# Kernel tuning notes

Measured on AMD Instinct MI355X. Metric: run time of the kernel, lower is better.

The kernel has to match this reference:

```python
import jax, jax.numpy as jnp
import numpy as np

V = 512          # vocab_size (= input_size = hidden_size of LSTMCell)
L = 128          # formula_max_len
PAD_ID = 0
SOS_ID = 1


def setup_inputs() -> dict:
    key = jax.random.key(0)
    k1, k2, k3, k4, k5 = jax.random.split(key, 5)
    B = 512
    s = 1.0 / np.sqrt(V)  # torch LSTMCell init scale
    return {
        "x": jax.random.normal(k1, (B, V), dtype=jnp.float32),
        "W_ih": jax.random.uniform(k2, (4 * V, V), jnp.float32, -s, s),
        "W_hh": jax.random.uniform(k3, (4 * V, V), jnp.float32, -s, s),
        "b_ih": jax.random.uniform(k4, (4 * V,), jnp.float32, -s, s),
        "b_hh": jax.random.uniform(k5, (4 * V,), jnp.float32, -s, s),
    }


def _decode(x, W_ih, W_hh, b_ih, b_hh):
    B = x.shape[0]
    dt = x.dtype
    sos = jax.nn.one_hot(SOS_ID, V, dtype=dt)
    pad = jax.nn.one_hot(PAD_ID, V, dtype=dt)

    h0 = x                      # hidden_state = x.squeeze()
    c0 = jnp.zeros_like(x)
    inp0 = jnp.broadcast_to(sos, (B, V))

    def step(carry, _):
        h, c, inp = carry
        # torch LSTMCell: gates = x W_ih^T + b_ih + h W_hh^T + b_hh, order i,f,g,o
        gates = inp @ W_ih.T + b_ih + h @ W_hh.T + b_hh   # [B, 4V]
        i, f, g, o = jnp.split(gates, 4, axis=-1)
        c_new = jax.nn.sigmoid(f) * c + jax.nn.sigmoid(i) * jnp.tanh(g)
        h_new = jax.nn.sigmoid(o) * jnp.tanh(c_new)
        probas = jax.nn.softmax(h_new, axis=-1)           # [B, V]
        nxt = jax.nn.one_hot(jnp.argmax(probas, axis=-1), V, dtype=dt)
        return (h_new, c_new, nxt), probas

    _, probas_seq = jax.lax.scan(step, (h0, c0, inp0), None, length=L - 1)
    # probas_seq: [L-1, B, V] -> [B, L-1, V]; last position stays PAD one-hot
    preds = jnp.swapaxes(probas_seq, 0, 1)
    pad_row = jnp.broadcast_to(pad, (B, 1, V))
    return jnp.concatenate([preds, pad_row], axis=1)      # [B, L, V]


def reference(x, W_ih, W_hh, b_ih, b_hh):
    return _decode(x, W_ih, W_hh, b_ih, b_hh)
```

## Files before the change

kernel.cpp:

```cpp
#include <hip/hip_runtime.h>

#define VSZ 512
#define LSEQ 128
#define NTHR 512
#define NBLK 256
#define NGRP 8
#define GBLK 32
#define SPIN_MAX  (1u << 20)
#define SPIN_STEP (1u << 17)

using short8  = __attribute__((ext_vector_type(8))) short;
using short4v = __attribute__((ext_vector_type(4))) short;
using floatx4 = __attribute__((ext_vector_type(4))) float;
using ull2v   = __attribute__((ext_vector_type(2))) unsigned long long;

static __device__ __forceinline__ short f2bf(float f) {
    union { float f; unsigned u; } v; v.f = f;
    unsigned u = v.u;
    unsigned r = (u + 0x7fffu + ((u >> 16) & 1u)) >> 16;
    return (short)r;
}
static __device__ __forceinline__ float bf2f(short s) {
    union { unsigned u; float f; } v; v.u = ((unsigned)(unsigned short)s) << 16;
    return v.f;
}
static __device__ __forceinline__ float fast_rcp(float x) { return __builtin_amdgcn_rcpf(x); }
static __device__ __forceinline__ float sigm(float x)   { return fast_rcp(1.0f + __expf(-x)); }
static __device__ __forceinline__ float tanh_f(float x) { return 1.0f - 2.0f * fast_rcp(__expf(2.0f * x) + 1.0f); }

template<bool F> static __device__ __forceinline__ void ldx4f(floatx4& d, const float* p) {
    if constexpr (F) asm volatile("global_load_dwordx4 %0, %1, off sc0"     : "=v"(d) : "v"(p));
    else             asm volatile("global_load_dwordx4 %0, %1, off sc0 sc1" : "=v"(d) : "v"(p));
}
template<bool F> static __device__ __forceinline__ void ldx4u(ull2v& d, const unsigned long long* p) {
    if constexpr (F) asm volatile("global_load_dwordx4 %0, %1, off sc0"     : "=v"(d) : "v"(p));
    else             asm volatile("global_load_dwordx4 %0, %1, off sc0 sc1" : "=v"(d) : "v"(p));
}
template<bool F> static __device__ __forceinline__ void ldx4s(short8& d, const short* p) {
    if constexpr (F) asm volatile("global_load_dwordx4 %0, %1, off sc0"     : "=v"(d) : "v"(p));
    else             asm volatile("global_load_dwordx4 %0, %1, off sc0 sc1" : "=v"(d) : "v"(p));
}
template<bool F> static __device__ __forceinline__ void stg16(void* p, unsigned v) {
    if constexpr (F) asm volatile("global_store_short %0, %1, off sc0"     :: "v"(p), "v"(v) : "memory");
    else             asm volatile("global_store_short %0, %1, off sc0 sc1" :: "v"(p), "v"(v) : "memory");
}
template<bool F> static __device__ __forceinline__ void stg32(void* p, unsigned v) {
    if constexpr (F) asm volatile("global_store_dword %0, %1, off sc0"     :: "v"(p), "v"(v) : "memory");
    else             asm volatile("global_store_dword %0, %1, off sc0 sc1" :: "v"(p), "v"(v) : "memory");
}
template<bool F> static __device__ __forceinline__ void stg64(void* p, unsigned long long v) {
    if constexpr (F) asm volatile("global_store_dwordx2 %0, %1, off sc0"     :: "v"(p), "v"(v) : "memory");
    else             asm volatile("global_store_dwordx2 %0, %1, off sc0 sc1" :: "v"(p), "v"(v) : "memory");
}

static __device__ __forceinline__ unsigned atomic_add_dev(unsigned* p, unsigned v) {
    unsigned old;
    asm volatile("global_atomic_add %0, %1, %2, off sc0 sc1\n\ts_waitcnt vmcnt(0)"
                 : "=v"(old) : "v"(p), "v"(v) : "memory");
    return old;
}
static __device__ __forceinline__ unsigned ld_dev_u32(const unsigned* p) {
    unsigned v;
    asm volatile("global_load_dword %0, %1, off sc0 sc1\n\ts_waitcnt vmcnt(0)"
                 : "=v"(v) : "v"(p) : "memory");
    return v;
}

static __device__ __forceinline__ void step_arrive(unsigned* cnt, int tid) {
    asm volatile("s_waitcnt vmcnt(0)" ::: "memory");
    __builtin_amdgcn_s_barrier();
    if (tid == 0) atomic_add_dev(cnt, 1u);
}
static __device__ __forceinline__ void step_wait(unsigned* cnt, int t, int tid) {
    if (tid == 0) {
        const unsigned target = (unsigned)(GBLK * (t + 1));
        unsigned it = 0;
        while (ld_dev_u32(cnt) < target) {
            if (++it > SPIN_STEP) break;
            if (it > 16) __builtin_amdgcn_s_sleep(1);
        }
    }
    __builtin_amdgcn_s_barrier();
}

static __device__ __forceinline__ void grid_barrier_dev(unsigned* ctrl, int tid, int bid) {
    asm volatile("s_waitcnt vmcnt(0)" ::: "memory");
    __builtin_amdgcn_s_barrier();
    if (tid == 0) {
        unsigned* l1   = ctrl + 256 + (bid >> 4) * 32;
        unsigned* root = ctrl + 768;
        unsigned* gen  = ctrl + 800;
        unsigned old = atomic_add_dev(l1, 1u);
        if ((old & 15) == 15) {
            unsigned rold = atomic_add_dev(root, 1u);
            if ((rold & 15) == 15) atomic_add_dev(gen, 1u);
        }
        unsigned it = 0;
        while (ld_dev_u32(gen) < 1u) {
            if (++it > SPIN_MAX) break;
            __builtin_amdgcn_s_sleep(1);
        }
    }
    __builtin_amdgcn_s_barrier();
}

__global__ void prep_wb(const float* __restrict__ Whh, short* __restrict__ Wb) {
    int tid = threadIdx.x;
    int lane = tid & 63;
    int T = blockIdx.x * 8 + (tid >> 6);
    int g  = T & 3;
    int k  = (T >> 2) & 15;
    int vt = T >> 6;
    int l15 = lane & 15, lg = lane >> 4;
    const float* src = Whh + (size_t)(g * 512 + vt * 16 + l15) * 512 + k * 32 + lg * 8;
    short8 o;
#pragma unroll
    for (int i = 0; i < 8; ++i) o[i] = f2bf(src[i]);
    *(short8*)(Wb + (size_t)T * 512 + lane * 8) = o;
}

__global__ void prep_wxb(const float* __restrict__ Wih, const float* __restrict__ bih,
                         const float* __restrict__ bhh, short* __restrict__ Wxb) {
    __shared__ float tile[64][65];
    int j0 = blockIdx.x * 64;
    int a0 = blockIdx.y * 64;
    int tid = threadIdx.x;
    for (int i = tid; i < 4096; i += NTHR) {
        int r = i >> 6, c = i & 63;
        int jj = j0 + r;
        tile[r][c] = Wih[(size_t)jj * 512 + a0 + c] + bih[jj] + bhh[jj];
    }
    __syncthreads();
    int v0 = j0 & 511;
    for (int i = tid; i < 4096; i += NTHR) {
        int r = i >> 6, c = i & 63;
        Wxb[(((size_t)(a0 + r)) * 512 + v0 + c) * 4 + (j0 >> 9)] = f2bf(tile[c][r]);
    }
}

template<bool F>
static __device__ __forceinline__ void run_decoder(
    const float* __restrict__ x, const short* __restrict__ Wb, const short* __restrict__ Wxb,
    float* __restrict__ out,
    short* hbuf, float* psum, unsigned long long* pmax, unsigned* cnt,
    short (*hlds)[520], float (*gl)[4][17], float* rinvL, int* aidL,
    int tid, int g, int j) {

    const int lane = tid & 63;
    const int w    = tid >> 6;
    const int l15  = lane & 15;
    const int lg   = lane >> 4;
    const int v16  = tid & 15;
    const int rr   = tid >> 4;
    const int row0g = g * 64;
    const int jv   = j * 16 + v16;
    const int mt = w >> 1, g0 = (w & 1) * 2;

    short8 bb[16][2];
#pragma unroll
    for (int kc = 0; kc < 16; ++kc) {
        const short* p = Wb + ((size_t)j * 64 + kc * 4 + g0) * 512 + lane * 8;
        asm volatile("global_load_dwordx4 %0, %1, off"             : "=v"(bb[kc][0]) : "v"(p));
        asm volatile("global_load_dwordx4 %0, %1, off offset:1024" : "=v"(bb[kc][1]) : "v"(p));
    }
    asm volatile("s_waitcnt vmcnt(0)" ::: "memory");
    __builtin_amdgcn_sched_barrier(0);

    float cst[2] = {0.f, 0.f};
    float exv[2] = {0.f, 0.f};

    for (int t = 0; t < LSEQ - 1; ++t) {
        if (t == 0) {
            if (tid < 64) aidL[tid] = 1;
#pragma unroll
            for (int p = 0; p < 8; ++p) {
                int row = (tid >> 6) + 8 * p;
                const float* src = x + (size_t)(row0g + row) * VSZ + (tid & 63) * 8;
                short8 v;
#pragma unroll
                for (int e = 0; e < 8; ++e) v[e] = f2bf(src[e]);
                *(short8*)&hlds[row][(tid & 63) * 8] = v;
            }
        } else {
            const int tb2 = (t + 1) & 1;
            floatx4 s4v; ull2v m2a, m2b;
            const float* ps = psum + ((size_t)tb2 * 512 + row0g) * 32 + tid * 4;
            const unsigned long long* pm = pmax + ((size_t)tb2 * 512 + row0g) * 32 + tid * 4;
            ldx4f<F>(s4v, ps);
            ldx4u<F>(m2a, pm);
            ldx4u<F>(m2b, pm + 2);
            short8 stg[8];
            const short* hsrc = hbuf + (size_t)tb2 * (VSZ * VSZ);
#pragma unroll
            for (int p = 0; p < 8; ++p) {
                int row = (tid >> 6) + 8 * p;
                ldx4s<F>(stg[p], hsrc + (size_t)(row0g + row) * VSZ + (tid & 63) * 8);
            }
            asm volatile("s_waitcnt vmcnt(8)" ::: "memory");
            __builtin_amdgcn_sched_barrier(0);
            float s = (s4v[0] + s4v[1]) + (s4v[2] + s4v[3]);
            unsigned long long m = m2a[0] > m2a[1] ? m2a[0] : m2a[1];
            unsigned long long m2 = m2b[0] > m2b[1] ? m2b[0] : m2b[1];
            if (m2 > m) m = m2;
#pragma unroll
            for (int d = 1; d < 8; d <<= 1) {
                s += __shfl_xor(s, d);
                unsigned long long mo = __shfl_xor(m, d);
                if (mo > m) m = mo;
            }
            if ((tid & 7) == 0) {
                int r = tid >> 3;
                rinvL[r] = 1.0f / s;
                aidL[r]  = (int)(~(unsigned)m);
            }
            asm volatile("s_waitcnt vmcnt(0)" ::: "memory");
            __builtin_amdgcn_sched_barrier(0);
#pragma unroll
            for (int p = 0; p < 8; ++p) {
                int row = (tid >> 6) + 8 * p;
                *(short8*)&hlds[row][(tid & 63) * 8] = stg[p];
            }
        }
        __syncthreads();

        short4v wxv0, wxv1;
        {
            const short* gp0 = Wxb + ((size_t)aidL[rr]      * VSZ + jv) * 4;
            const short* gp1 = Wxb + ((size_t)aidL[rr + 32] * VSZ + jv) * 4;
            asm volatile("global_load_dwordx2 %0, %1, off" : "=v"(wxv0) : "v"(gp0));
            asm volatile("global_load_dwordx2 %0, %1, off" : "=v"(wxv1) : "v"(gp1));
        }

        floatx4 a0v = {0,0,0,0}, a1v = {0,0,0,0};
#pragma unroll
        for (int kc = 0; kc < 16; ++kc) {
            short8 av = *(const short8*)&hlds[mt * 16 + l15][kc * 32 + lg * 8];
            a0v = __builtin_amdgcn_mfma_f32_16x16x32_bf16(av, bb[kc][0], a0v, 0, 0, 0);
            a1v = __builtin_amdgcn_mfma_f32_16x16x32_bf16(av, bb[kc][1], a1v, 0, 0, 0);
        }
#pragma unroll
        for (int q = 0; q < 4; ++q) {
            gl[mt * 16 + lg * 4 + q][g0][l15]     = a0v[q];
            gl[mt * 16 + lg * 4 + q][g0 + 1][l15] = a1v[q];
        }
        __syncthreads();

        asm volatile("s_waitcnt vmcnt(0)" ::: "memory");
        __builtin_amdgcn_sched_barrier(0);
        float pex0 = exv[0], pex1 = exv[1];
#pragma unroll
        for (int s2 = 0; s2 < 2; ++s2) {
            int r = rr + 32 * s2;
            short4v wxv = s2 ? wxv1 : wxv0;
            float gi = gl[r][0][v16] + bf2f(wxv[0]);
            float gf = gl[r][1][v16] + bf2f(wxv[1]);
            float gg = gl[r][2][v16] + bf2f(wxv[2]);
            float go = gl[r][3][v16] + bf2f(wxv[3]);
            float cn = sigm(gf) * cst[s2] + sigm(gi) * tanh_f(gg);
            cst[s2] = cn;
            float hn = sigm(go) * tanh_f(cn);
            stg16<F>(hbuf + (size_t)(t & 1) * (VSZ * VSZ) + (size_t)(row0g + r) * VSZ + jv,
                     (unsigned)(unsigned short)f2bf(hn));
            float e = __expf(hn);
            exv[s2] = e;
            float s = e; float mv = e; int mi = jv;
#pragma unroll
            for (int m = 1; m < 16; m <<= 1) {
                s += __shfl_xor(s, m);
                float mv2 = __shfl_xor(mv, m);
                int   mi2 = __shfl_xor(mi, m);
                if (mv2 > mv || (mv2 == mv && mi2 < mi)) { mv = mv2; mi = mi2; }
            }
            if (v16 == 0) {
                size_t o32 = ((size_t)(t & 1) * 512 + row0g + r) * 32 + j;
                unsigned long long pk =
                    ((unsigned long long)__float_as_uint(mv) << 32) | (unsigned)(~(unsigned)mi);
                stg32<F>(psum + o32, __float_as_uint(s));
                stg64<F>(pmax + o32, pk);
            }
        }

        step_arrive(cnt, tid);
        if (t > 0) {
            __builtin_nontemporal_store(pex0 * rinvL[rr],
                &out[((size_t)(row0g + rr) * LSEQ + (t - 1)) * VSZ + jv]);
            __builtin_nontemporal_store(pex1 * rinvL[rr + 32],
                &out[((size_t)(row0g + rr + 32) * LSEQ + (t - 1)) * VSZ + jv]);
        }
        step_wait(cnt, t, tid);
    }

    {
        floatx4 s4v;
        ldx4f<F>(s4v, psum + (size_t)row0g * 32 + tid * 4);
        asm volatile("s_waitcnt vmcnt(0)" ::: "memory");
        __builtin_amdgcn_sched_barrier(0);
        float s = (s4v[0] + s4v[1]) + (s4v[2] + s4v[3]);
#pragma unroll
        for (int d = 1; d < 8; d <<= 1) s += __shfl_xor(s, d);
        if ((tid & 7) == 0) rinvL[tid >> 3] = 1.0f / s;
    }
    __syncthreads();
#pragma unroll
    for (int s2 = 0; s2 < 2; ++s2) {
        int r = rr + 32 * s2;
        __builtin_nontemporal_store(exv[s2] * rinvL[r],
            &out[((size_t)(row0g + r) * LSEQ + (LSEQ - 2)) * VSZ + jv]);
        __builtin_nontemporal_store((jv == 0) ? 1.0f : 0.0f,
            &out[((size_t)(row0g + r) * LSEQ + (LSEQ - 1)) * VSZ + jv]);
    }
}

__launch_bounds__(NTHR, 2)
__global__ void decoder_coop(const float* __restrict__ x, const short* __restrict__ Wb,
                             const short* __restrict__ Wxb,
                             short* hbuf_s, float* psum_s, unsigned long long* pmax_s,
                             short* hbuf_f, float* psum_f, unsigned long long* pmax_f,
                             unsigned* ctrl, float* __restrict__ out, int allow_fast) {
    __shared__ short hlds[64][520];
    __shared__ float gl[64][4][17];
    __shared__ float rinvL[64];
    __shared__ int   aidL[64];
    __shared__ int   sh_xcc, sh_slot, sh_ok;
    __shared__ unsigned sh_cnts[NGRP];

    const int tid = threadIdx.x;
    const int bid = blockIdx.x;

    if (tid == 0) {
        unsigned xcc;
        asm volatile("s_getreg_b32 %0, hwreg(HW_REG_XCC_ID)" : "=s"(xcc));
        xcc &= 7;
        unsigned slot = atomic_add_dev(ctrl + xcc * 32, 1u);
        sh_xcc = (int)xcc; sh_slot = (int)slot;
    }
    grid_barrier_dev(ctrl, tid, bid);
    if (tid < NGRP) sh_cnts[tid] = ld_dev_u32(ctrl + tid * 32);
    __syncthreads();
    if (tid == 0) {
        int ok = allow_fast && (sh_slot < GBLK);
#pragma unroll
        for (int g = 0; g < NGRP; ++g) ok = ok && (sh_cnts[g] == GBLK);
        sh_ok = ok;
    }
    __syncthreads();
    const int ok = sh_ok;
    const int g = ok ? sh_xcc : (bid & 7);
    const int j = ok ? sh_slot : (bid >> 3);
    unsigned* cnt = ctrl + 1024 + g * 64;

    if (ok)
        run_decoder<true >(x, Wb, Wxb, out, hbuf_f, psum_f, pmax_f, cnt,
                           hlds, gl, rinvL, aidL, tid, g, j);
    else
        run_decoder<false>(x, Wb, Wxb, out, hbuf_s, psum_s, pmax_s, cnt,
                           hlds, gl, rinvL, aidL, tid, g, j);
}

extern "C" void kernel_launch(void* const* d_in, const int* in_sizes, int n_in,
                              void* d_out, int out_size, void* d_ws, size_t ws_size,
                              hipStream_t stream) {
    const float* x    = (const float*)d_in[0];
    const float* W_ih = (const float*)d_in[1];
    const float* W_hh = (const float*)d_in[2];
    const float* b_ih = (const float*)d_in[3];
    const float* b_hh = (const float*)d_in[4];

    char* ws = (char*)d_ws;
    short* Wb     = (short*)ws;
    short* Wxb    = (short*)(ws + (2u << 20));
    short* hbuf_s = (short*)(ws + (4u << 20));
    float* psum_s = (float*)(ws + (5u << 20));
    unsigned long long* pmax_s = (unsigned long long*)(ws + (5u << 20) + (128u << 10));
    unsigned* ctrl = (unsigned*)(ws + (5u << 20) + (384u << 10));
    short* hbuf_f = (short*)(ws + (5u << 20) + (400u << 10));
    float* psum_f = (float*)(ws + (6u << 20) + (400u << 10));
    unsigned long long* pmax_f = (unsigned long long*)(ws + (6u << 20) + (528u << 10));
    const size_t needed = (6ull << 20) + (784ull << 10);
    int allow_fast = (ws_size >= needed) ? 1 : 0;

    prep_wb<<<256, NTHR, 0, stream>>>(W_hh, Wb);
    prep_wxb<<<dim3(32, 8), NTHR, 0, stream>>>(W_ih, b_ih, b_hh, Wxb);
    hipMemsetAsync(ctrl, 0, 16384, stream);

    float* outp = (float*)d_out;
    void* args[] = { (void*)&x, (void*)&Wb, (void*)&Wxb,
                     (void*)&hbuf_s, (void*)&psum_s, (void*)&pmax_s,
                     (void*)&hbuf_f, (void*)&psum_f, (void*)&pmax_f,
                     (void*)&ctrl, (void*)&outp, (void*)&allow_fast };
    hipLaunchCooperativeKernel((const void*)decoder_coop, dim3(NBLK), dim3(NTHR),
                               args, 0, stream);
}
```

Baseline: 639.0 us.

## Add 256-thread, 512-block decoder variant with 16 row groups per step

```diff
diff --git a/kernel.cpp b/kernel.cpp
--- a/kernel.cpp
+++ b/kernel.cpp
@@ -2,9 +2,7 @@
 
 #define VSZ 512
 #define LSEQ 128
-#define NTHR 512
-#define NBLK 256
-#define NGRP 8
+#define PREPTHR 512
 #define GBLK 32
 #define SPIN_MAX  (1u << 20)
 #define SPIN_STEP (1u << 17)
@@ -83,17 +81,18 @@
     __builtin_amdgcn_s_barrier();
 }
 
+template<int NL1>
 static __device__ __forceinline__ void grid_barrier_dev(unsigned* ctrl, int tid, int bid) {
     asm volatile("s_waitcnt vmcnt(0)" ::: "memory");
     __builtin_amdgcn_s_barrier();
     if (tid == 0) {
         unsigned* l1   = ctrl + 256 + (bid >> 4) * 32;
-        unsigned* root = ctrl + 768;
-        unsigned* gen  = ctrl + 800;
+        unsigned* root = ctrl + 256 + NL1 * 32;
+        unsigned* gen  = root + 32;
         unsigned old = atomic_add_dev(l1, 1u);
         if ((old & 15) == 15) {
             unsigned rold = atomic_add_dev(root, 1u);
-            if ((rold & 15) == 15) atomic_add_dev(gen, 1u);
+            if ((rold & (NL1 - 1)) == (unsigned)(NL1 - 1)) atomic_add_dev(gen, 1u);
         }
         unsigned it = 0;
         while (ld_dev_u32(gen) < 1u) {
@@ -125,21 +124,21 @@
     int j0 = blockIdx.x * 64;
     int a0 = blockIdx.y * 64;
     int tid = threadIdx.x;
-    for (int i = tid; i < 4096; i += NTHR) {
+    for (int i = tid; i < 4096; i += PREPTHR) {
         int r = i >> 6, c = i & 63;
         int jj = j0 + r;
         tile[r][c] = Wih[(size_t)jj * 512 + a0 + c] + bih[jj] + bhh[jj];
     }
     __syncthreads();
     int v0 = j0 & 511;
-    for (int i = tid; i < 4096; i += NTHR) {
+    for (int i = tid; i < 4096; i += PREPTHR) {
         int r = i >> 6, c = i & 63;
         Wxb[(((size_t)(a0 + r)) * 512 + v0 + c) * 4 + (j0 >> 9)] = f2bf(tile[c][r]);
     }
 }
 
 template<bool F>
-static __device__ __forceinline__ void run_decoder(
+static __device__ __forceinline__ void run_decoder512(
     const float* __restrict__ x, const short* __restrict__ Wb, const short* __restrict__ Wxb,
     float* __restrict__ out,
     short* hbuf, float* psum, unsigned long long* pmax, unsigned* cnt,
@@ -311,18 +310,18 @@
     }
 }
 
-__launch_bounds__(NTHR, 2)
-__global__ void decoder_coop(const float* __restrict__ x, const short* __restrict__ Wb,
-                             const short* __restrict__ Wxb,
-                             short* hbuf_s, float* psum_s, unsigned long long* pmax_s,
-                             short* hbuf_f, float* psum_f, unsigned long long* pmax_f,
-                             unsigned* ctrl, float* __restrict__ out, int allow_fast) {
+__launch_bounds__(512, 2)
+__global__ void decoder_coop512(const float* __restrict__ x, const short* __restrict__ Wb,
+                                const short* __restrict__ Wxb,
+                                short* hbuf_s, float* psum_s, unsigned long long* pmax_s,
+                                short* hbuf_f, float* psum_f, unsigned long long* pmax_f,
+                                unsigned* ctrl, float* __restrict__ out, int allow_fast) {
     __shared__ short hlds[64][520];
     __shared__ float gl[64][4][17];
     __shared__ float rinvL[64];
     __shared__ int   aidL[64];
     __shared__ int   sh_xcc, sh_slot, sh_ok;
-    __shared__ unsigned sh_cnts[NGRP];
+    __shared__ unsigned sh_cnts[8];
 
     const int tid = threadIdx.x;
     const int bid = blockIdx.x;
@@ -334,27 +333,246 @@
         unsigned slot = atomic_add_dev(ctrl + xcc * 32, 1u);
         sh_xcc = (int)xcc; sh_slot = (int)slot;
     }
-    grid_barrier_dev(ctrl, tid, bid);
-    if (tid < NGRP) sh_cnts[tid] = ld_dev_u32(ctrl + tid * 32);
+    grid_barrier_dev<16>(ctrl, tid, bid);
+    if (tid < 8) sh_cnts[tid] = ld_dev_u32(ctrl + tid * 32);
     __syncthreads();
     if (tid == 0) {
         int ok = allow_fast && (sh_slot < GBLK);
 #pragma unroll
-        for (int g = 0; g < NGRP; ++g) ok = ok && (sh_cnts[g] == GBLK);
+        for (int g = 0; g < 8; ++g) ok = ok && (sh_cnts[g] == GBLK);
         sh_ok = ok;
     }
     __syncthreads();
     const int ok = sh_ok;
     const int g = ok ? sh_xcc : (bid & 7);
     const int j = ok ? sh_slot : (bid >> 3);
-    unsigned* cnt = ctrl + 1024 + g * 64;
+    unsigned* cnt = ctrl + 2048 + g * 64;
 
     if (ok)
-        run_decoder<true >(x, Wb, Wxb, out, hbuf_f, psum_f, pmax_f, cnt,
-                           hlds, gl, rinvL, aidL, tid, g, j);
+        run_decoder512<true >(x, Wb, Wxb, out, hbuf_f, psum_f, pmax_f, cnt,
+                              hlds, gl, rinvL, aidL, tid, g, j);
     else
-        run_decoder<false>(x, Wb, Wxb, out, hbuf_s, psum_s, pmax_s, cnt,
-                           hlds, gl, rinvL, aidL, tid, g, j);
+        run_decoder512<false>(x, Wb, Wxb, out, hbuf_s, psum_s, pmax_s, cnt,
+                              hlds, gl, rinvL, aidL, tid, g, j);
+}
+
+template<bool F>
+static __device__ __forceinline__ void run_decoder256(
+    const float* __restrict__ x, const short* __restrict__ Wb, const short* __restrict__ Wxb,
+    float* __restrict__ out,
+    short* hbuf, float* psum, unsigned long long* pmax, unsigned* cnt,
+    short (*hlds)[520], float (*gl)[4][17], float* rinvL, int* aidL,
+    int tid, int g, int j) {
+
+    const int lane = tid & 63;
+    const int w    = tid >> 6;
+    const int l15  = lane & 15;
+    const int lg   = lane >> 4;
+    const int v16  = tid & 15;
+    const int rr   = tid >> 4;
+    const int row0g = g * 32;
+    const int jv   = j * 16 + v16;
+    const int mt = w >> 1, g0 = (w & 1) * 2;
+
+    short8 bb[16][2];
+#pragma unroll
+    for (int kc = 0; kc < 16; ++kc) {
+        const short* p = Wb + ((size_t)j * 64 + kc * 4 + g0) * 512 + lane * 8;
+        asm volatile("global_load_dwordx4 %0, %1, off"             : "=v"(bb[kc][0]) : "v"(p));
+        asm volatile("global_load_dwordx4 %0, %1, off offset:1024" : "=v"(bb[kc][1]) : "v"(p));
+    }
+    asm volatile("s_waitcnt vmcnt(0)" ::: "memory");
+    __builtin_amdgcn_sched_barrier(0);
+
+    float cst[2] = {0.f, 0.f};
+    float exv[2] = {0.f, 0.f};
+
+    for (int t = 0; t < LSEQ - 1; ++t) {
+        if (t == 0) {
+            if (tid < 32) aidL[tid] = 1;
+#pragma unroll
+            for (int p = 0; p < 8; ++p) {
+                int row = (tid >> 6) + 4 * p;
+                const float* src = x + (size_t)(row0g + row) * VSZ + (tid & 63) * 8;
+                short8 v;
+#pragma unroll
+                for (int e = 0; e < 8; ++e) v[e] = f2bf(src[e]);
+                *(short8*)&hlds[row][(tid & 63) * 8] = v;
+            }
+        } else {
+            const int tb2 = (t + 1) & 1;
+            floatx4 s4v; ull2v m2a, m2b;
+            const float* ps = psum + ((size_t)tb2 * 512 + row0g) * 32 + tid * 4;
+            const unsigned long long* pm = pmax + ((size_t)tb2 * 512 + row0g) * 32 + tid * 4;
+            ldx4f<F>(s4v, ps);
+            ldx4u<F>(m2a, pm);
+            ldx4u<F>(m2b, pm + 2);
+            short8 stg[8];
+            const short* hsrc = hbuf + (size_t)tb2 * (VSZ * VSZ);
+#pragma unroll
+            for (int p = 0; p < 8; ++p) {
+                int row = (tid >> 6) + 4 * p;
+                ldx4s<F>(stg[p], hsrc + (size_t)(row0g + row) * VSZ + (tid & 63) * 8);
+            }
+            asm volatile("s_waitcnt vmcnt(8)" ::: "memory");
+            __builtin_amdgcn_sched_barrier(0);
+            float s = (s4v[0] + s4v[1]) + (s4v[2] + s4v[3]);
+            unsigned long long m = m2a[0] > m2a[1] ? m2a[0] : m2a[1];
+            unsigned long long m2 = m2b[0] > m2b[1] ? m2b[0] : m2b[1];
+            if (m2 > m) m = m2;
+#pragma unroll
+            for (int d = 1; d < 8; d <<= 1) {
+                s += __shfl_xor(s, d);
+                unsigned long long mo = __shfl_xor(m, d);
+                if (mo > m) m = mo;
+            }
+            if ((tid & 7) == 0) {
+                int r = tid >> 3;
+                rinvL[r] = 1.0f / s;
+                aidL[r]  = (int)(~(unsigned)m);
+            }
+            asm volatile("s_waitcnt vmcnt(0)" ::: "memory");
+            __builtin_amdgcn_sched_barrier(0);
+#pragma unroll
+            for (int p = 0; p < 8; ++p) {
+                int row = (tid >> 6) + 4 * p;
+                *(short8*)&hlds[row][(tid & 63) * 8] = stg[p];
+            }
+        }
+        __syncthreads();
+
+        short4v wxv0, wxv1;
+        {
+            const short* gp0 = Wxb + ((size_t)aidL[rr]      * VSZ + jv) * 4;
+            const short* gp1 = Wxb + ((size_t)aidL[rr + 16] * VSZ + jv) * 4;
+            asm volatile("global_load_dwordx2 %0, %1, off" : "=v"(wxv0) : "v"(gp0));
+            asm volatile("global_load_dwordx2 %0, %1, off" : "=v"(wxv1) : "v"(gp1));
+        }
+
+        floatx4 a0v = {0,0,0,0}, a1v = {0,0,0,0};
+#pragma unroll
+        for (int kc = 0; kc < 16; ++kc) {
+            short8 av = *(const short8*)&hlds[mt * 16 + l15][kc * 32 + lg * 8];
+            a0v = __builtin_amdgcn_mfma_f32_16x16x32_bf16(av, bb[kc][0], a0v, 0, 0, 0);
+            a1v = __builtin_amdgcn_mfma_f32_16x16x32_bf16(av, bb[kc][1], a1v, 0, 0, 0);
+        }
+#pragma unroll
+        for (int q = 0; q < 4; ++q) {
+            gl[mt * 16 + lg * 4 + q][g0][l15]     = a0v[q];
+            gl[mt * 16 + lg * 4 + q][g0 + 1][l15] = a1v[q];
+        }
+        __syncthreads();
+
+        asm volatile("s_waitcnt vmcnt(0)" ::: "memory");
+        __builtin_amdgcn_sched_barrier(0);
+        float pex0 = exv[0], pex1 = exv[1];
+#pragma unroll
+        for (int s2 = 0; s2 < 2; ++s2) {
+            int r = rr + 16 * s2;
+            short4v wxv = s2 ? wxv1 : wxv0;
+            float gi = gl[r][0][v16] + bf2f(wxv[0]);
+            float gf = gl[r][1][v16] + bf2f(wxv[1]);
+            float gg = gl[r][2][v16] + bf2f(wxv[2]);
+            float go = gl[r][3][v16] + bf2f(wxv[3]);
+            float cn = sigm(gf) * cst[s2] + sigm(gi) * tanh_f(gg);
+            cst[s2] = cn;
+            float hn = sigm(go) * tanh_f(cn);
+            stg16<F>(hbuf + (size_t)(t & 1) * (VSZ * VSZ) + (size_t)(row0g + r) * VSZ + jv,
+                     (unsigned)(unsigned short)f2bf(hn));
+            float e = __expf(hn);
+            exv[s2] = e;
+            float s = e; float mv = e; int mi = jv;
+#pragma unroll
+            for (int m = 1; m < 16; m <<= 1) {
+                s += __shfl_xor(s, m);
+                float mv2 = __shfl_xor(mv, m);
+                int   mi2 = __shfl_xor(mi, m);
+                if (mv2 > mv || (mv2 == mv && mi2 < mi)) { mv = mv2; mi = mi2; }
+            }
+            if (v16 == 0) {
+                size_t o32 = ((size_t)(t & 1) * 512 + row0g + r) * 32 + j;
+                unsigned long long pk =
+                    ((unsigned long long)__float_as_uint(mv) << 32) | (unsigned)(~(unsigned)mi);
+                stg32<F>(psum + o32, __float_as_uint(s));
+                stg64<F>(pmax + o32, pk);
+            }
+        }
+
+        step_arrive(cnt, tid);
+        if (t > 0) {
+            __builtin_nontemporal_store(pex0 * rinvL[rr],
+                &out[((size_t)(row0g + rr) * LSEQ + (t - 1)) * VSZ + jv]);
+            __builtin_nontemporal_store(pex1 * rinvL[rr + 16],
+                &out[((size_t)(row0g + rr + 16) * LSEQ + (t - 1)) * VSZ + jv]);
+        }
+        step_wait(cnt, t, tid);
+    }
+
+    {
+        floatx4 s4v;
+        ldx4f<F>(s4v, psum + (size_t)row0g * 32 + tid * 4);
+        asm volatile("s_waitcnt vmcnt(0)" ::: "memory");
+        __builtin_amdgcn_sched_barrier(0);
+        float s = (s4v[0] + s4v[1]) + (s4v[2] + s4v[3]);
+#pragma unroll
+        for (int d = 1; d < 8; d <<= 1) s += __shfl_xor(s, d);
+        if ((tid & 7) == 0) rinvL[tid >> 3] = 1.0f / s;
+    }
+    __syncthreads();
+#pragma unroll
+    for (int s2 = 0; s2 < 2; ++s2) {
+        int r = rr + 16 * s2;
+        __builtin_nontemporal_store(exv[s2] * rinvL[r],
+            &out[((size_t)(row0g + r) * LSEQ + (LSEQ - 2)) * VSZ + jv]);
+        __builtin_nontemporal_store((jv == 0) ? 1.0f : 0.0f,
+            &out[((size_t)(row0g + r) * LSEQ + (LSEQ - 1)) * VSZ + jv]);
+    }
+}
+
+__launch_bounds__(256, 2)
+__global__ void decoder_coop256(const float* __restrict__ x, const short* __restrict__ Wb,
+                                const short* __restrict__ Wxb,
+                                short* hbuf_s, float* psum_s, unsigned long long* pmax_s,
+                                short* hbuf_f, float* psum_f, unsigned long long* pmax_f,
+                                unsigned* ctrl, float* __restrict__ out, int allow_fast) {
+    __shared__ short hlds[32][520];
+    __shared__ float gl[32][4][17];
+    __shared__ float rinvL[32];
+    __shared__ int   aidL[32];
+    __shared__ int   sh_xcc, sh_slot, sh_ok;
+    __shared__ unsigned sh_cnts[8];
+
+    const int tid = threadIdx.x;
+    const int bid = blockIdx.x;
+
+    if (tid == 0) {
+        unsigned xcc;
+        asm volatile("s_getreg_b32 %0, hwreg(HW_REG_XCC_ID)" : "=s"(xcc));
+        xcc &= 7;
+        unsigned slot = atomic_add_dev(ctrl + xcc * 32, 1u);
+        sh_xcc = (int)xcc; sh_slot = (int)slot;
+    }
+    grid_barrier_dev<32>(ctrl, tid, bid);
+    if (tid < 8) sh_cnts[tid] = ld_dev_u32(ctrl + tid * 32);
+    __syncthreads();
+    if (tid == 0) {
+        int ok = allow_fast && (sh_slot < 2 * GBLK);
+#pragma unroll
+        for (int g = 0; g < 8; ++g) ok = ok && (sh_cnts[g] == 2 * GBLK);
+        sh_ok = ok;
+    }
+    __syncthreads();
+    const int ok = sh_ok;
+    const int g = ok ? (sh_xcc * 2 + (sh_slot >> 5)) : (bid & 15);
+    const int j = ok ? (sh_slot & 31) : ((bid >> 4) & 31);
+    unsigned* cnt = ctrl + 2048 + g * 64;
+
+    if (ok)
+        run_decoder256<true >(x, Wb, Wxb, out, hbuf_f, psum_f, pmax_f, cnt,
+                              hlds, gl, rinvL, aidL, tid, g, j);
+    else
+        run_decoder256<false>(x, Wb, Wxb, out, hbuf_s, psum_s, pmax_s, cnt,
+                              hlds, gl, rinvL, aidL, tid, g, j);
 }
 
 extern "C" void kernel_launch(void* const* d_in, const int* in_sizes, int n_in,
@@ -379,15 +597,24 @@
     const size_t needed = (6ull << 20) + (784ull << 10);
     int allow_fast = (ws_size >= needed) ? 1 : 0;
 
-    prep_wb<<<256, NTHR, 0, stream>>>(W_hh, Wb);
-    prep_wxb<<<dim3(32, 8), NTHR, 0, stream>>>(W_ih, b_ih, b_hh, Wxb);
+    prep_wb<<<256, PREPTHR, 0, stream>>>(W_hh, Wb);
+    prep_wxb<<<dim3(32, 8), PREPTHR, 0, stream>>>(W_ih, b_ih, b_hh, Wxb);
     hipMemsetAsync(ctrl, 0, 16384, stream);
+
+    int nb256 = 0;
+    hipError_t qerr = hipOccupancyMaxActiveBlocksPerMultiprocessor(
+        &nb256, (const void*)decoder_coop256, 256, 0);
+    const int use256 = (qerr == hipSuccess && nb256 >= 2);
 
     float* outp = (float*)d_out;
     void* args[] = { (void*)&x, (void*)&Wb, (void*)&Wxb,
                      (void*)&hbuf_s, (void*)&psum_s, (void*)&pmax_s,
                      (void*)&hbuf_f, (void*)&psum_f, (void*)&pmax_f,
                      (void*)&ctrl, (void*)&outp, (void*)&allow_fast };
-    hipLaunchCooperativeKernel((const void*)decoder_coop, dim3(NBLK), dim3(NTHR),
-                               args, 0, stream);
-}
+    if (use256)
+        hipLaunchCooperativeKernel((const void*)decoder_coop256, dim3(512), dim3(256),
+                                   args, 0, stream);
+    else
+        hipLaunchCooperativeKernel((const void*)decoder_coop512, dim3(256), dim3(512),
+                                   args, 0, stream);
+}
```

New measurement: 658.6 us. 3.1% more time.

## Split each group's 64 rows into two independent chains to overlap barrier waits

Applied to the files above, without the earlier changes.

```diff
diff --git a/kernel.cpp b/kernel.cpp
--- a/kernel.cpp
+++ b/kernel.cpp
@@ -139,65 +139,51 @@
 }
 
 template<bool F>
-static __device__ __forceinline__ void run_decoder(
-    const float* __restrict__ x, const short* __restrict__ Wb, const short* __restrict__ Wxb,
-    float* __restrict__ out,
-    short* hbuf, float* psum, unsigned long long* pmax, unsigned* cnt,
+static __device__ __forceinline__ void chain_phase(
+    int t, const float* __restrict__ x, const short* __restrict__ Wxb,
+    short* hbuf, float* psum, unsigned long long* pmax,
     short (*hlds)[520], float (*gl)[4][17], float* rinvL, int* aidL,
-    int tid, int g, int j) {
+    const short8 (&bb)[16], float& cst, float& exv, float& pex,
+    int tid, int row0c, int jv, int j, int mt, int gate) {
 
     const int lane = tid & 63;
-    const int w    = tid >> 6;
     const int l15  = lane & 15;
     const int lg   = lane >> 4;
     const int v16  = tid & 15;
     const int rr   = tid >> 4;
-    const int row0g = g * 64;
-    const int jv   = j * 16 + v16;
-    const int mt = w >> 1, g0 = (w & 1) * 2;
-
-    short8 bb[16][2];
-#pragma unroll
-    for (int kc = 0; kc < 16; ++kc) {
-        const short* p = Wb + ((size_t)j * 64 + kc * 4 + g0) * 512 + lane * 8;
-        asm volatile("global_load_dwordx4 %0, %1, off"             : "=v"(bb[kc][0]) : "v"(p));
-        asm volatile("global_load_dwordx4 %0, %1, off offset:1024" : "=v"(bb[kc][1]) : "v"(p));
-    }
-    asm volatile("s_waitcnt vmcnt(0)" ::: "memory");
-    __builtin_amdgcn_sched_barrier(0);
-
-    float cst[2] = {0.f, 0.f};
-    float exv[2] = {0.f, 0.f};
-
-    for (int t = 0; t < LSEQ - 1; ++t) {
-        if (t == 0) {
-            if (tid < 64) aidL[tid] = 1;
-#pragma unroll
-            for (int p = 0; p < 8; ++p) {
-                int row = (tid >> 6) + 8 * p;
-                const float* src = x + (size_t)(row0g + row) * VSZ + (tid & 63) * 8;
-                short8 v;
-#pragma unroll
-                for (int e = 0; e < 8; ++e) v[e] = f2bf(src[e]);
-                *(short8*)&hlds[row][(tid & 63) * 8] = v;
-            }
-        } else {
-            const int tb2 = (t + 1) & 1;
-            floatx4 s4v; ull2v m2a, m2b;
-            const float* ps = psum + ((size_t)tb2 * 512 + row0g) * 32 + tid * 4;
-            const unsigned long long* pm = pmax + ((size_t)tb2 * 512 + row0g) * 32 + tid * 4;
+
+    if (t == 0) {
+        if (tid < 32) aidL[tid] = 1;
+#pragma unroll
+        for (int p = 0; p < 4; ++p) {
+            int row = (tid >> 6) + 8 * p;
+            const float* src = x + (size_t)(row0c + row) * VSZ + (tid & 63) * 8;
+            short8 v;
+#pragma unroll
+            for (int e = 0; e < 8; ++e) v[e] = f2bf(src[e]);
+            *(short8*)&hlds[row][(tid & 63) * 8] = v;
+        }
+    } else {
+        const int tb2 = (t + 1) & 1;
+        floatx4 s4v; ull2v m2a, m2b;
+        const bool red = tid < 256;
+        if (red) {
+            const float* ps = psum + ((size_t)tb2 * 512 + row0c) * 32 + tid * 4;
+            const unsigned long long* pm = pmax + ((size_t)tb2 * 512 + row0c) * 32 + tid * 4;
             ldx4f<F>(s4v, ps);
             ldx4u<F>(m2a, pm);
             ldx4u<F>(m2b, pm + 2);
-            short8 stg[8];
-            const short* hsrc = hbuf + (size_t)tb2 * (VSZ * VSZ);
-#pragma unroll
-            for (int p = 0; p < 8; ++p) {
-                int row = (tid >> 6) + 8 * p;
-                ldx4s<F>(stg[p], hsrc + (size_t)(row0g + row) * VSZ + (tid & 63) * 8);
-            }
-            asm volatile("s_waitcnt vmcnt(8)" ::: "memory");
-            __builtin_amdgcn_sched_barrier(0);
+        }
+        short8 stg[4];
+        const short* hsrc = hbuf + (size_t)tb2 * (VSZ * VSZ);
+#pragma unroll
+        for (int p = 0; p < 4; ++p) {
+            int row = (tid >> 6) + 8 * p;
+            ldx4s<F>(stg[p], hsrc + (size_t)(row0c + row) * VSZ + (tid & 63) * 8);
+        }
+        asm volatile("s_waitcnt vmcnt(4)" ::: "memory");
+        __builtin_amdgcn_sched_barrier(0);
+        if (red) {
             float s = (s4v[0] + s4v[1]) + (s4v[2] + s4v[3]);
             unsigned long long m = m2a[0] > m2a[1] ? m2a[0] : m2a[1];
             unsigned long long m2 = m2b[0] > m2b[1] ? m2b[0] : m2b[1];
@@ -213,102 +199,140 @@
                 rinvL[r] = 1.0f / s;
                 aidL[r]  = (int)(~(unsigned)m);
             }
-            asm volatile("s_waitcnt vmcnt(0)" ::: "memory");
-            __builtin_amdgcn_sched_barrier(0);
-#pragma unroll
-            for (int p = 0; p < 8; ++p) {
-                int row = (tid >> 6) + 8 * p;
-                *(short8*)&hlds[row][(tid & 63) * 8] = stg[p];
-            }
-        }
-        __syncthreads();
-
-        short4v wxv0, wxv1;
-        {
-            const short* gp0 = Wxb + ((size_t)aidL[rr]      * VSZ + jv) * 4;
-            const short* gp1 = Wxb + ((size_t)aidL[rr + 32] * VSZ + jv) * 4;
-            asm volatile("global_load_dwordx2 %0, %1, off" : "=v"(wxv0) : "v"(gp0));
-            asm volatile("global_load_dwordx2 %0, %1, off" : "=v"(wxv1) : "v"(gp1));
-        }
-
-        floatx4 a0v = {0,0,0,0}, a1v = {0,0,0,0};
-#pragma unroll
-        for (int kc = 0; kc < 16; ++kc) {
-            short8 av = *(const short8*)&hlds[mt * 16 + l15][kc * 32 + lg * 8];
-            a0v = __builtin_amdgcn_mfma_f32_16x16x32_bf16(av, bb[kc][0], a0v, 0, 0, 0);
-            a1v = __builtin_amdgcn_mfma_f32_16x16x32_bf16(av, bb[kc][1], a1v, 0, 0, 0);
-        }
-#pragma unroll
-        for (int q = 0; q < 4; ++q) {
-            gl[mt * 16 + lg * 4 + q][g0][l15]     = a0v[q];
-            gl[mt * 16 + lg * 4 + q][g0 + 1][l15] = a1v[q];
-        }
-        __syncthreads();
-
+        }
         asm volatile("s_waitcnt vmcnt(0)" ::: "memory");
         __builtin_amdgcn_sched_barrier(0);
-        float pex0 = exv[0], pex1 = exv[1];
-#pragma unroll
-        for (int s2 = 0; s2 < 2; ++s2) {
-            int r = rr + 32 * s2;
-            short4v wxv = s2 ? wxv1 : wxv0;
-            float gi = gl[r][0][v16] + bf2f(wxv[0]);
-            float gf = gl[r][1][v16] + bf2f(wxv[1]);
-            float gg = gl[r][2][v16] + bf2f(wxv[2]);
-            float go = gl[r][3][v16] + bf2f(wxv[3]);
-            float cn = sigm(gf) * cst[s2] + sigm(gi) * tanh_f(gg);
-            cst[s2] = cn;
-            float hn = sigm(go) * tanh_f(cn);
-            stg16<F>(hbuf + (size_t)(t & 1) * (VSZ * VSZ) + (size_t)(row0g + r) * VSZ + jv,
-                     (unsigned)(unsigned short)f2bf(hn));
-            float e = __expf(hn);
-            exv[s2] = e;
-            float s = e; float mv = e; int mi = jv;
-#pragma unroll
-            for (int m = 1; m < 16; m <<= 1) {
-                s += __shfl_xor(s, m);
-                float mv2 = __shfl_xor(mv, m);
-                int   mi2 = __shfl_xor(mi, m);
-                if (mv2 > mv || (mv2 == mv && mi2 < mi)) { mv = mv2; mi = mi2; }
-            }
-            if (v16 == 0) {
-                size_t o32 = ((size_t)(t & 1) * 512 + row0g + r) * 32 + j;
-                unsigned long long pk =
-                    ((unsigned long long)__float_as_uint(mv) << 32) | (unsigned)(~(unsigned)mi);
-                stg32<F>(psum + o32, __float_as_uint(s));
-                stg64<F>(pmax + o32, pk);
-            }
-        }
-
-        step_arrive(cnt, tid);
-        if (t > 0) {
-            __builtin_nontemporal_store(pex0 * rinvL[rr],
-                &out[((size_t)(row0g + rr) * LSEQ + (t - 1)) * VSZ + jv]);
-            __builtin_nontemporal_store(pex1 * rinvL[rr + 32],
-                &out[((size_t)(row0g + rr + 32) * LSEQ + (t - 1)) * VSZ + jv]);
-        }
-        step_wait(cnt, t, tid);
-    }
-
+#pragma unroll
+        for (int p = 0; p < 4; ++p) {
+            int row = (tid >> 6) + 8 * p;
+            *(short8*)&hlds[row][(tid & 63) * 8] = stg[p];
+        }
+    }
+    __syncthreads();
+
+    short4v wxv;
     {
-        floatx4 s4v;
-        ldx4f<F>(s4v, psum + (size_t)row0g * 32 + tid * 4);
+        const short* gp = Wxb + ((size_t)aidL[rr] * VSZ + jv) * 4;
+        asm volatile("global_load_dwordx2 %0, %1, off" : "=v"(wxv) : "v"(gp));
+    }
+
+    floatx4 acc = {0, 0, 0, 0};
+#pragma unroll
+    for (int kc = 0; kc < 16; ++kc) {
+        short8 av = *(const short8*)&hlds[mt * 16 + l15][kc * 32 + lg * 8];
+        acc = __builtin_amdgcn_mfma_f32_16x16x32_bf16(av, bb[kc], acc, 0, 0, 0);
+    }
+#pragma unroll
+    for (int q = 0; q < 4; ++q)
+        gl[mt * 16 + lg * 4 + q][gate][l15] = acc[q];
+    __syncthreads();
+
+    asm volatile("s_waitcnt vmcnt(0)" ::: "memory");
+    __builtin_amdgcn_sched_barrier(0);
+    pex = exv;
+    {
+        float gi = gl[rr][0][v16] + bf2f(wxv[0]);
+        float gf = gl[rr][1][v16] + bf2f(wxv[1]);
+        float gg = gl[rr][2][v16] + bf2f(wxv[2]);
+        float go = gl[rr][3][v16] + bf2f(wxv[3]);
+        float cn = sigm(gf) * cst + sigm(gi) * tanh_f(gg);
+        cst = cn;
+        float hn = sigm(go) * tanh_f(cn);
+        stg16<F>(hbuf + (size_t)(t & 1) * (VSZ * VSZ) + (size_t)(row0c + rr) * VSZ + jv,
+                 (unsigned)(unsigned short)f2bf(hn));
+        float e = __expf(hn);
+        exv = e;
+        float s = e; float mv = e; int mi = jv;
+#pragma unroll
+        for (int m = 1; m < 16; m <<= 1) {
+            s += __shfl_xor(s, m);
+            float mv2 = __shfl_xor(mv, m);
+            int   mi2 = __shfl_xor(mi, m);
+            if (mv2 > mv || (mv2 == mv && mi2 < mi)) { mv = mv2; mi = mi2; }
+        }
+        if (v16 == 0) {
+            size_t o32 = ((size_t)(t & 1) * 512 + row0c + rr) * 32 + j;
+            unsigned long long pk =
+                ((unsigned long long)__float_as_uint(mv) << 32) | (unsigned)(~(unsigned)mi);
+            stg32<F>(psum + o32, __float_as_uint(s));
+            stg64<F>(pmax + o32, pk);
+        }
+    }
+}
+
+template<bool F>
+static __device__ __forceinline__ void run_decoder(
+    const float* __restrict__ x, const short* __restrict__ Wb, const short* __restrict__ Wxb,
+    float* __restrict__ out,
+    short* hbuf, float* psum, unsigned long long* pmax,
+    unsigned* cntA, unsigned* cntB,
+    short (*hldsA)[520], short (*hldsB)[520],
+    float (*glA)[4][17], float (*glB)[4][17],
+    float* rinvA, float* rinvB, int* aidA, int* aidB,
+    int tid, int g, int j) {
+
+    const int lane = tid & 63;
+    const int w    = tid >> 6;
+    const int v16  = tid & 15;
+    const int rr   = tid >> 4;
+    const int jv   = j * 16 + v16;
+    const int mt   = w >> 2;
+    const int gate = w & 3;
+    const int row0A = g * 64;
+    const int row0B = g * 64 + 32;
+
+    short8 bb[16];
+#pragma unroll
+    for (int kc = 0; kc < 16; ++kc) {
+        const short* p = Wb + ((size_t)j * 64 + kc * 4 + gate) * 512 + lane * 8;
+        asm volatile("global_load_dwordx4 %0, %1, off" : "=v"(bb[kc]) : "v"(p));
+    }
+    asm volatile("s_waitcnt vmcnt(0)" ::: "memory");
+    __builtin_amdgcn_sched_barrier(0);
+
+    float cstA = 0.f, cstB = 0.f, exvA = 0.f, exvB = 0.f, pexA = 0.f, pexB = 0.f;
+
+    for (int t = 0; t < LSEQ - 1; ++t) {
+        if (t > 0) step_wait(cntA, t - 1, tid);
+        chain_phase<F>(t, x, Wxb, hbuf, psum, pmax, hldsA, glA, rinvA, aidA,
+                       bb, cstA, exvA, pexA, tid, row0A, jv, j, mt, gate);
+        step_arrive(cntA, tid);
+        if (t > 0)
+            __builtin_nontemporal_store(pexA * rinvA[rr],
+                &out[((size_t)(row0A + rr) * LSEQ + (t - 1)) * VSZ + jv]);
+
+        if (t > 0) step_wait(cntB, t - 1, tid);
+        chain_phase<F>(t, x, Wxb, hbuf, psum, pmax, hldsB, glB, rinvB, aidB,
+                       bb, cstB, exvB, pexB, tid, row0B, jv, j, mt, gate);
+        step_arrive(cntB, tid);
+        if (t > 0)
+            __builtin_nontemporal_store(pexB * rinvB[rr],
+                &out[((size_t)(row0B + rr) * LSEQ + (t - 1)) * VSZ + jv]);
+    }
+
+    step_wait(cntA, LSEQ - 2, tid);
+    step_wait(cntB, LSEQ - 2, tid);
+    if (tid < 256) {
+        floatx4 sA, sB;
+        ldx4f<F>(sA, psum + (size_t)row0A * 32 + tid * 4);
+        ldx4f<F>(sB, psum + (size_t)row0B * 32 + tid * 4);
         asm volatile("s_waitcnt vmcnt(0)" ::: "memory");
         __builtin_amdgcn_sched_barrier(0);
-        float s = (s4v[0] + s4v[1]) + (s4v[2] + s4v[3]);
-#pragma unroll
-        for (int d = 1; d < 8; d <<= 1) s += __shfl_xor(s, d);
-        if ((tid & 7) == 0) rinvL[tid >> 3] = 1.0f / s;
-    }
-    __syncthreads();
-#pragma unroll
-    for (int s2 = 0; s2 < 2; ++s2) {
-        int r = rr + 32 * s2;
-        __builtin_nontemporal_store(exv[s2] * rinvL[r],
-            &out[((size_t)(row0g + r) * LSEQ + (LSEQ - 2)) * VSZ + jv]);
-        __builtin_nontemporal_store((jv == 0) ? 1.0f : 0.0f,
-            &out[((size_t)(row0g + r) * LSEQ + (LSEQ - 1)) * VSZ + jv]);
-    }
+        float a = (sA[0] + sA[1]) + (sA[2] + sA[3]);
+        float b = (sB[0] + sB[1]) + (sB[2] + sB[3]);
+#pragma unroll
+        for (int d = 1; d < 8; d <<= 1) { a += __shfl_xor(a, d); b += __shfl_xor(b, d); }
+        if ((tid & 7) == 0) { rinvA[tid >> 3] = 1.0f / a; rinvB[tid >> 3] = 1.0f / b; }
+    }
+    __syncthreads();
+    __builtin_nontemporal_store(exvA * rinvA[rr],
+        &out[((size_t)(row0A + rr) * LSEQ + (LSEQ - 2)) * VSZ + jv]);
+    __builtin_nontemporal_store((jv == 0) ? 1.0f : 0.0f,
+        &out[((size_t)(row0A + rr) * LSEQ + (LSEQ - 1)) * VSZ + jv]);
+    __builtin_nontemporal_store(exvB * rinvB[rr],
+        &out[((size_t)(row0B + rr) * LSEQ + (LSEQ - 2)) * VSZ + jv]);
+    __builtin_nontemporal_store((jv == 0) ? 1.0f : 0.0f,
+        &out[((size_t)(row0B + rr) * LSEQ + (LSEQ - 1)) * VSZ + jv]);
 }
 
 __launch_bounds__(NTHR, 2)
@@ -317,10 +341,10 @@
                              short* hbuf_s, float* psum_s, unsigned long long* pmax_s,
                              short* hbuf_f, float* psum_f, unsigned long long* pmax_f,
                              unsigned* ctrl, float* __restrict__ out, int allow_fast) {
-    __shared__ short hlds[64][520];
-    __shared__ float gl[64][4][17];
-    __shared__ float rinvL[64];
-    __shared__ int   aidL[64];
+    __shared__ short hlds[2][32][520];
+    __shared__ float gl[2][32][4][17];
+    __shared__ float rinvL[2][32];
+    __shared__ int   aidL[2][32];
     __shared__ int   sh_xcc, sh_slot, sh_ok;
     __shared__ unsigned sh_cnts[NGRP];
 
@@ -347,14 +371,17 @@
     const int ok = sh_ok;
     const int g = ok ? sh_xcc : (bid & 7);
     const int j = ok ? sh_slot : (bid >> 3);
-    unsigned* cnt = ctrl + 1024 + g * 64;
+    unsigned* cntA = ctrl + 1024 + (g * 2 + 0) * 64;
+    unsigned* cntB = ctrl + 1024 + (g * 2 + 1) * 64;
 
     if (ok)
-        run_decoder<true >(x, Wb, Wxb, out, hbuf_f, psum_f, pmax_f, cnt,
-                           hlds, gl, rinvL, aidL, tid, g, j);
+        run_decoder<true >(x, Wb, Wxb, out, hbuf_f, psum_f, pmax_f, cntA, cntB,
+                           hlds[0], hlds[1], gl[0], gl[1],
+                           rinvL[0], rinvL[1], aidL[0], aidL[1], tid, g, j);
     else
-        run_decoder<false>(x, Wb, Wxb, out, hbuf_s, psum_s, pmax_s, cnt,
-                           hlds, gl, rinvL, aidL, tid, g, j);
+        run_decoder<false>(x, Wb, Wxb, out, hbuf_s, psum_s, pmax_s, cntA, cntB,
+                           hlds[0], hlds[1], gl[0], gl[1],
+                           rinvL[0], rinvL[1], aidL[0], aidL[1], tid, g, j);
 }
 
 extern "C" void kernel_launch(void* const* d_in, const int* in_sizes, int n_in,
```

Result: slower. 732.4 us (+14.6%).
